# Kernel tuning notes

Hardware: AMD Instinct MI355X
Metric: run time of the kernel (lower is better)

The kernel has to match this reference:

```python
import jax, jax.numpy as jnp
import numpy as np

B, S, DIM = 1, 2048, 1024
HEADS, KV_HEADS, DH = 16, 2, 64
GQ = HEADS // KV_HEADS
CBS = 64   # compress block size
SBS = 64   # selection block size
NUM_SEL = 8
WIN = 512  # sliding window size
NUM_MEM = 1
SCALE = DH ** -0.5
NEG = -jnp.finfo(jnp.float32).max


def setup_inputs():
    ks = jax.random.split(jax.random.key(0), 12)
    cdim = CBS * DH
    dim_inner = HEADS * DH
    dim_kv = KV_HEADS * DH
    p = lambda k, shape: jax.random.normal(k, shape, jnp.float32) * 0.02
    return {
        "x": jax.random.normal(ks[0], (B, S, DIM), jnp.float32),
        "rms_g": jnp.ones((DIM,), jnp.float32),
        "W_qkv": p(ks[1], (DIM, dim_inner + 2 * dim_kv)),
        "k_pos": p(ks[2], (KV_HEADS, CBS, DH)),
        "v_pos": p(ks[3], (KV_HEADS, CBS, DH)),
        "mem_kv": p(ks[4], (2, KV_HEADS, NUM_MEM, DH)),
        "kW1": p(ks[5], (cdim, cdim)), "kb1": jnp.zeros((cdim,), jnp.float32),
        "kW2": p(ks[6], (cdim, DH)), "kb2": jnp.zeros((DH,), jnp.float32),
        "vW1": p(ks[7], (cdim, cdim)), "vb1": jnp.zeros((cdim,), jnp.float32),
        "vW2": p(ks[8], (cdim, DH)), "vb2": jnp.zeros((DH,), jnp.float32),
        "W_comb": p(ks[9], (DIM, 3 * HEADS)),
        "b_comb": jnp.tile(jnp.array([-2.0, -2.0, 2.0], jnp.float32), HEADS),
        "W_out": p(ks[10], (HEADS * DH, DIM)),
    }


def _rot_half(u):
    v = u.reshape(u.shape[:-1] + (DH // 2, 2))
    return jnp.stack([-v[..., 1], v[..., 0]], axis=-1).reshape(u.shape)


def reference(x, rms_g, W_qkv, k_pos, v_pos, mem_kv, kW1, kb1, kW2, kb2,
              vW1, vb1, vW2, vb2, W_comb, b_comb, W_out):
    n_cb = S // CBS
    n_fb = S // SBS
    num_sel = min(NUM_SEL, n_cb)

    # RMSNorm
    xn = x * jax.lax.rsqrt(jnp.mean(x * x, -1, keepdims=True) + jnp.finfo(jnp.float32).eps) * rms_g

    qkv = xn @ W_qkv
    q, k, v = jnp.split(qkv, [HEADS * DH, (HEADS + KV_HEADS) * DH], axis=-1)
    q = q.reshape(B, S, HEADS, DH).transpose(0, 2, 1, 3)       # b h n d
    k = k.reshape(B, S, KV_HEADS, DH).transpose(0, 2, 1, 3)
    v = v.reshape(B, S, KV_HEADS, DH).transpose(0, 2, 1, 3)

    # ---- compressed branch: per-block MLP compression of K/V ----
    kc = (k + jnp.tile(k_pos, (1, n_cb, 1))[None]).reshape(B, KV_HEADS, n_cb, CBS * DH)
    vc = (v + jnp.tile(v_pos, (1, n_cb, 1))[None]).reshape(B, KV_HEADS, n_cb, CBS * DH)
    ck = jax.nn.relu(kc @ kW1 + kb1) @ kW2 + kb2               # b h w d
    cv = jax.nn.relu(vc @ vW1 + vb1) @ vW2 + vb2
    ck = jnp.concatenate([jnp.broadcast_to(mem_kv[0], (B, KV_HEADS, NUM_MEM, DH)), ck], axis=2)
    cv = jnp.concatenate([jnp.broadcast_to(mem_kv[1], (B, KV_HEADS, NUM_MEM, DH)), cv], axis=2)
    ck_seq = jnp.concatenate([jnp.full((NUM_MEM,), -1), (jnp.arange(n_cb) + 1) * CBS - 1])
    cmask = ck_seq[None, :] < jnp.arange(S)[:, None]           # [S, mem+n_cb]
    qg = q.reshape(B, KV_HEADS, GQ, S, DH)
    csim = jnp.einsum('bhgid,bhjd->bhgij', qg, ck) * SCALE
    csim = jnp.where(cmask, csim, NEG)
    c_out = jnp.einsum('bhgij,bhjd->bhgid', jax.nn.softmax(csim, -1), cv).reshape(B, HEADS, S, DH)

    # ---- rotary embedding (interleaved pairs, theta=10000) ----
    inv_freq = 1.0 / (10000.0 ** (jnp.arange(0, DH, 2, dtype=jnp.float32) / DH))
    freqs = jnp.repeat(jnp.arange(S, dtype=jnp.float32)[:, None] * inv_freq, 2, axis=-1)
    cos, sin = jnp.cos(freqs), jnp.sin(freqs)
    rq = q * cos + _rot_half(q) * sin
    rk = k * cos + _rot_half(k) * sin

    # ---- block selection from compressed attention scores ----
    imp = csim[..., NUM_MEM:].mean(axis=2)                     # mean over grouped queries: [B,KVH,S,n_cb]
    imp = jnp.concatenate([jnp.full(imp.shape[:-1] + (1,), -1000.0), imp], -1)
    imp = jax.nn.softmax(imp, -1)[..., 1:]
    sel_val, sel_idx = jax.lax.top_k(imp, num_sel)             # [B,KVH,S,sel]
    fmask = jnp.broadcast_to((sel_val > 1e-10)[..., None], (B, KV_HEADS, S, num_sel, SBS))
    diag_idx = jnp.broadcast_to((jnp.arange(S) // SBS)[None, None, :, None], (B, KV_HEADS, S, 1))
    sel_idx = jnp.concatenate([sel_idx, diag_idx], -1)         # append own (diagonal) block
    causal = jnp.tril(jnp.ones((SBS, SBS), bool))
    diag_mask = jnp.broadcast_to(jnp.tile(causal, (n_fb, 1))[None, None, :, None, :], (B, KV_HEADS, S, 1, SBS))
    fmask = jnp.concatenate([fmask, diag_mask], axis=-2).reshape(B, KV_HEADS, S, (num_sel + 1) * SBS)

    # ---- fine attention over gathered selected blocks ----
    fkb = rk.reshape(B, KV_HEADS, 1, n_fb, SBS, DH)
    fvb = v.reshape(B, KV_HEADS, 1, n_fb, SBS, DH)
    gi = sel_idx[..., None, None]                              # [B,KVH,S,sel+1,1,1]
    fk = jnp.take_along_axis(fkb, gi, axis=3).reshape(B, KV_HEADS, S, (num_sel + 1) * SBS, DH)
    fv = jnp.take_along_axis(fvb, gi, axis=3).reshape(B, KV_HEADS, S, (num_sel + 1) * SBS, DH)
    fqg = rq.reshape(B, KV_HEADS, GQ, S, DH)
    fsim = jnp.einsum('bhgid,bhijd->bhgij', fqg, fk) * SCALE
    fsim = jnp.where(fmask[:, :, None], fsim, NEG)
    f_out = jnp.einsum('bhgij,bhijd->bhgid', jax.nn.softmax(fsim, -1), fv).reshape(B, HEADS, S, DH)

    # ---- causal sliding window (exact window, look_backward=1) ----
    skf = jnp.repeat(rk, GQ, axis=1)
    svf = jnp.repeat(v, GQ, axis=1)
    nw = S // WIN
    kw = skf.reshape(B, HEADS, nw, WIN, DH)
    vw = svf.reshape(B, HEADS, nw, WIN, DH)
    kcat = jnp.concatenate([jnp.pad(kw, ((0, 0), (0, 0), (1, 0), (0, 0), (0, 0)))[:, :, :nw], kw], axis=3)
    vcat = jnp.concatenate([jnp.pad(vw, ((0, 0), (0, 0), (1, 0), (0, 0), (0, 0)))[:, :, :nw], vw], axis=3)
    qw = rq.reshape(B, HEADS, nw, WIN, DH)
    gq_pos = jnp.arange(nw)[:, None, None] * WIN + jnp.arange(WIN)[None, :, None]
    gk_pos = jnp.arange(nw)[:, None, None] * WIN - WIN + jnp.arange(2 * WIN)[None, None, :]
    smask = (gk_pos >= 0) & (gk_pos <= gq_pos) & (gq_pos - gk_pos <= WIN)
    ssim = jnp.where(smask, jnp.einsum('bhwid,bhwjd->bhwij', qw, kcat) * SCALE, NEG)
    s_out = jnp.einsum('bhwij,bhwjd->bhwid', jax.nn.softmax(ssim, -1), vcat).reshape(B, HEADS, S, DH)

    # ---- learned per-token, per-head strategy combination ----
    gates = jax.nn.sigmoid(xn @ W_comb + b_comb).reshape(B, S, HEADS, 3).transpose(0, 2, 1, 3)
    out = gates[..., 0:1] * c_out + gates[..., 1:2] * f_out + gates[..., 2:3] * s_out
    return out.transpose(0, 2, 1, 3).reshape(B, S, HEADS * DH) @ W_out
```

## Files before the change

### kernel.cpp

```cpp
#include <hip/hip_runtime.h>
#include <hip/hip_bf16.h>
#include <cstddef>
#include <cstdint>

#define S      2048
#define DIM    1024
#define HEADS  16
#define KVH    2
#define GQ     8
#define DH     64
#define CBS    64
#define SBS    64
#define NUMSEL 8
#define WIN    512
#define NCB    (S / CBS)
#define CDIM   (CBS * DH)
#define QKVC   (HEADS * DH + 2 * KVH * DH)
#define KOFF   (HEADS * DH)
#define VOFF   (HEADS * DH + KVH * DH)
#define SCALE  0.125f
#define RMS_EPS 1.1920928955078125e-07f

typedef __attribute__((ext_vector_type(8))) short bf16x8;
typedef __attribute__((ext_vector_type(4))) float f32x4;

__device__ inline short f2bs(float f) {
    __hip_bfloat16 b = __float2bfloat16(f);
    return *(short*)&b;
}

__device__ inline float wave_sum(float v) {
    for (int o = 32; o > 0; o >>= 1) v += __shfl_xor(v, o);
    return v;
}

__global__ __launch_bounds__(256) void rmsnorm_kernel(
        const float* __restrict__ x, const float* __restrict__ g,
        float* __restrict__ xn, __hip_bfloat16* __restrict__ xnb) {
    int s = blockIdx.x, tid = threadIdx.x;
    const float4* row = (const float4*)(x + (size_t)s * DIM);
    float4 v = row[tid];
    float ss = v.x * v.x + v.y * v.y + v.z * v.z + v.w * v.w;
    ss = wave_sum(ss);
    __shared__ float red[4];
    if ((tid & 63) == 0) red[tid >> 6] = ss;
    __syncthreads();
    float tot = red[0] + red[1] + red[2] + red[3];
    float sc = rsqrtf(tot / (float)DIM + RMS_EPS);
    float4 gg = ((const float4*)g)[tid];
    float4 o;
    o.x = v.x * sc * gg.x; o.y = v.y * sc * gg.y;
    o.z = v.z * sc * gg.z; o.w = v.w * sc * gg.w;
    ((float4*)(xn + (size_t)s * DIM))[tid] = o;
    size_t b = (size_t)s * DIM + tid * 4;
    xnb[b + 0] = __float2bfloat16(o.x);
    xnb[b + 1] = __float2bfloat16(o.y);
    xnb[b + 2] = __float2bfloat16(o.z);
    xnb[b + 3] = __float2bfloat16(o.w);
}

__global__ __launch_bounds__(256) void cast_bf16_kernel(
        const float* __restrict__ in, __hip_bfloat16* __restrict__ out, int n4) {
    int e = blockIdx.x * 256 + threadIdx.x;
    if (e >= n4) return;
    float4 v = ((const float4*)in)[e];
    out[4 * e + 0] = __float2bfloat16(v.x);
    out[4 * e + 1] = __float2bfloat16(v.y);
    out[4 * e + 2] = __float2bfloat16(v.z);
    out[4 * e + 3] = __float2bfloat16(v.w);
}

__global__ __launch_bounds__(256) void transpose_cast_kernel(
        const float* __restrict__ W, short* __restrict__ Wt, int K, int N) {
    __shared__ float tile[64][65];
    int n0 = blockIdx.x * 64, k0 = blockIdx.y * 64;
    int tid = threadIdx.x;
    #pragma unroll
    for (int e = 0; e < 16; e++) {
        int idx = tid + e * 256;
        int r = idx >> 6, c = idx & 63;
        float v = 0.f;
        if (n0 + c < N) v = W[(size_t)(k0 + r) * N + n0 + c];
        tile[r][c] = v;
    }
    __syncthreads();
    #pragma unroll
    for (int e = 0; e < 16; e++) {
        int idx = tid + e * 256;
        int r = idx >> 6, c = idx & 63;
        if (n0 + r < N)
            Wt[(size_t)(n0 + r) * K + k0 + c] = f2bs(tile[c][r]);
    }
}

__global__ __launch_bounds__(256) void transpose_v_kernel(
        const float* __restrict__ qkv, short* __restrict__ vtg) {
    int k0 = blockIdx.x * 64, kvh = blockIdx.y;
    __shared__ float tile[64][65];
    int tid = threadIdx.x;
    #pragma unroll
    for (int e = 0; e < 16; e++) {
        int idx = tid + e * 256;
        int key = idx >> 6, d = idx & 63;
        tile[key][d] = qkv[(size_t)(k0 + key) * QKVC + VOFF + kvh * DH + d];
    }
    __syncthreads();
    #pragma unroll
    for (int e = 0; e < 16; e++) {
        int idx = tid + e * 256;
        int d = idx >> 6, key = idx & 63;
        vtg[(size_t)(kvh * DH + d) * S + k0 + key] = f2bs(tile[key][d]);
    }
}

template <int BM, int BN, int WM, int WN, int ACT>
__global__ __launch_bounds__(256) void gemm_bt_kernel(
        const __hip_bfloat16* __restrict__ A, const short* __restrict__ Bt,
        const float* __restrict__ bias, float* __restrict__ C,
        int M, int N, int K) {
    constexpr int BK = 32;
    constexpr int TM = BM / (WM * 16);
    constexpr int TN = BN / (WN * 16);
    constexpr int LDK = BK + 8;
    __shared__ short As[BM][LDK];
    __shared__ short Bs[BN][LDK];
    int tid = threadIdx.x;
    int wave = tid >> 6, lane = tid & 63;
    int wm = wave % WM, wn = wave / WM;
    int m0 = wm * TM * 16, n0 = wn * TN * 16;
    int bm = blockIdx.y * BM, bn = blockIdx.x * BN;
    int lm = lane & 15, quad = lane >> 4;
    const short* Ash = (const short*)A;
    f32x4 acc[TM][TN] = {};
    for (int k0 = 0; k0 < K; k0 += BK) {
        #pragma unroll
        for (int e = 0; e < BM * BK / (256 * 8); e++) {
            int idx = (tid + e * 256) * 8;
            int r = idx >> 5, kk = idx & 31;
            *(bf16x8*)(&As[r][kk]) =
                *(const bf16x8*)(Ash + (size_t)(bm + r) * K + k0 + kk);
        }
        #pragma unroll
        for (int e = 0; e < BN * BK / (256 * 8); e++) {
            int idx = (tid + e * 256) * 8;
            int r = idx >> 5, kk = idx & 31;
            bf16x8 v = {};
            if (bn + r < N)
                v = *(const bf16x8*)(Bt + (size_t)(bn + r) * K + k0 + kk);
            *(bf16x8*)(&Bs[r][kk]) = v;
        }
        __syncthreads();
        bf16x8 af[TM], bf_[TN];
        #pragma unroll
        for (int i = 0; i < TM; i++)
            af[i] = *(const bf16x8*)(&As[m0 + i * 16 + lm][quad * 8]);
        #pragma unroll
        for (int j = 0; j < TN; j++)
            bf_[j] = *(const bf16x8*)(&Bs[n0 + j * 16 + lm][quad * 8]);
        #pragma unroll
        for (int i = 0; i < TM; i++)
            #pragma unroll
            for (int j = 0; j < TN; j++)
                acc[i][j] = __builtin_amdgcn_mfma_f32_16x16x32_bf16(
                    af[i], bf_[j], acc[i][j], 0, 0, 0);
        __syncthreads();
    }
    #pragma unroll
    for (int i = 0; i < TM; i++) {
        #pragma unroll
        for (int j = 0; j < TN; j++) {
            int gn = bn + n0 + j * 16 + lm;
            if (gn >= N) continue;
            #pragma unroll
            for (int r = 0; r < 4; r++) {
                int gm = bm + m0 + i * 16 + quad * 4 + r;
                float v = acc[i][j][r];
                if (bias) v += bias[gn];
                if (ACT == 2) v = 1.f / (1.f + expf(-v));
                C[(size_t)gm * N + gn] = v;
            }
        }
    }
}

template <int BM, int BN, int WM, int WN>
__global__ __launch_bounds__(256) void gemm_mfma_kernel(
        const __hip_bfloat16* __restrict__ A, const float* __restrict__ B,
        float* __restrict__ C, int M, int N, int K, int kslice) {
    constexpr int BK = 32;
    constexpr int TM = BM / (WM * 16);
    constexpr int TN = BN / (WN * 16);
    constexpr int LDK = BK + 8;
    constexpr int NB = BN * BK / 256;
    __shared__ __hip_bfloat16 As[BM][LDK];
    __shared__ __hip_bfloat16 Bs[BN][LDK];
    int tid = threadIdx.x;
    int wave = tid >> 6, lane = tid & 63;
    int wm = wave % WM, wn = wave / WM;
    int m0 = wm * TM * 16, n0 = wn * TN * 16;
    int bm = blockIdx.y * BM, bn = blockIdx.x * BN;
    int kbeg = blockIdx.z * kslice, kend = kbeg + kslice;
    int lm = lane & 15, quad = lane >> 4;
    f32x4 acc[TM][TN] = {};
    for (int k0 = kbeg; k0 < kend; k0 += BK) {
        #pragma unroll
        for (int e = 0; e < BM * BK / (256 * 8); e++) {
            int idx = (tid + e * 256) * 8;
            int r = idx >> 5, kk = idx & 31;
            *(bf16x8*)(&As[r][kk]) =
                *(const bf16x8*)(A + (size_t)(bm + r) * K + k0 + kk);
        }
        float tmpB[NB];
        #pragma unroll
        for (int e = 0; e < NB; e++) {
            int idx = tid + e * 256;
            int kk = idx / BN, n = idx % BN;
            tmpB[e] = B[(size_t)(k0 + kk) * N + bn + n];
        }
        #pragma unroll
        for (int e = 0; e < NB; e++) {
            int idx = tid + e * 256;
            int kk = idx / BN, n = idx % BN;
            Bs[n][kk] = __float2bfloat16(tmpB[e]);
        }
        __syncthreads();
        bf16x8 af[TM], bf_[TN];
        #pragma unroll
        for (int i = 0; i < TM; i++)
            af[i] = *(const bf16x8*)(&As[m0 + i * 16 + lm][quad * 8]);
        #pragma unroll
        for (int j = 0; j < TN; j++)
            bf_[j] = *(const bf16x8*)(&Bs[n0 + j * 16 + lm][quad * 8]);
        #pragma unroll
        for (int i = 0; i < TM; i++)
            #pragma unroll
            for (int j = 0; j < TN; j++)
                acc[i][j] = __builtin_amdgcn_mfma_f32_16x16x32_bf16(
                    af[i], bf_[j], acc[i][j], 0, 0, 0);
        __syncthreads();
    }
    size_t cbase = (size_t)blockIdx.z * M * N;
    #pragma unroll
    for (int i = 0; i < TM; i++) {
        #pragma unroll
        for (int j = 0; j < TN; j++) {
            int gn = bn + n0 + j * 16 + lm;
            #pragma unroll
            for (int r = 0; r < 4; r++) {
                int gm = bm + m0 + i * 16 + quad * 4 + r;
                C[cbase + (size_t)gm * N + gn] = acc[i][j][r];
            }
        }
    }
}

__global__ __launch_bounds__(256) void gemm_splitk_kernel(
        const float* __restrict__ A, const float* __restrict__ B,
        float* __restrict__ P, int M, int N, int K, int kslice) {
    const int BM = 64, BN = 64, BK = 16;
    __shared__ float As[BK][BM + 4];
    __shared__ float Bs[BK][BN];
    int bm = blockIdx.y * BM, bn = blockIdx.x * BN;
    int z = blockIdx.z;
    int kbeg = z * kslice, kend = kbeg + kslice;
    int tid = threadIdx.x;
    int tx = tid & 15, ty = tid >> 4;
    float acc[4][4] = {{0.f}};
    for (int k0 = kbeg; k0 < kend; k0 += BK) {
        #pragma unroll
        for (int e = 0; e < 4; e++) {
            int idx = tid + e * 256;
            int m = idx >> 4, kk = idx & 15;
            int gm = bm + m;
            As[kk][m] = (gm < M) ? A[(size_t)gm * K + k0 + kk] : 0.f;
        }
        #pragma unroll
        for (int e = 0; e < 4; e++) {
            int idx = tid + e * 256;
            int kk = idx >> 6, n = idx & 63;
            int gn = bn + n;
            Bs[kk][n] = (gn < N) ? B[(size_t)(k0 + kk) * N + gn] : 0.f;
        }
        __syncthreads();
        #pragma unroll
        for (int kk = 0; kk < BK; kk++) {
            float a[4], b[4];
            #pragma unroll
            for (int i = 0; i < 4; i++) a[i] = As[kk][ty * 4 + i];
            #pragma unroll
            for (int j = 0; j < 4; j++) b[j] = Bs[kk][tx * 4 + j];
            #pragma unroll
            for (int i = 0; i < 4; i++)
                #pragma unroll
                for (int j = 0; j < 4; j++) acc[i][j] += a[i] * b[j];
        }
        __syncthreads();
    }
    #pragma unroll
    for (int i = 0; i < 4; i++) {
        int gm = bm + ty * 4 + i;
        if (gm >= M) continue;
        #pragma unroll
        for (int j = 0; j < 4; j++) {
            int gn = bn + tx * 4 + j;
            if (gn >= N) continue;
            P[((size_t)z * M + gm) * N + gn] = acc[i][j];
        }
    }
}

template <int ACT>
__global__ __launch_bounds__(256) void reduce_splitk_kernel(
        const float* __restrict__ P, const float* __restrict__ bias,
        float* __restrict__ C, int MN, int N, int splits) {
    int e = blockIdx.x * 256 + threadIdx.x;
    if (e >= MN) return;
    float s = 0.f;
    for (int z = 0; z < splits; z++) s += P[(size_t)z * MN + e];
    s += bias[e % N];
    if (ACT == 1) s = fmaxf(s, 0.f);
    C[e] = s;
}

__global__ __launch_bounds__(256) void rotary_kernel(
        const float* __restrict__ qkv, short* __restrict__ rqb, short* __restrict__ rkb) {
    int s = blockIdx.x, tid = threadIdx.x;
    for (int p = tid; p < (HEADS + KVH) * (DH / 2); p += 256) {
        int t; const float* src; short* dst;
        if (p < HEADS * (DH / 2)) {
            int h = p >> 5; t = p & 31;
            src = qkv + (size_t)s * QKVC + h * DH + 2 * t;
            dst = rqb + (size_t)s * (HEADS * DH) + h * DH + 2 * t;
        } else {
            int pp = p - HEADS * (DH / 2);
            int h = pp >> 5; t = pp & 31;
            src = qkv + (size_t)s * QKVC + KOFF + h * DH + 2 * t;
            dst = rkb + (size_t)s * (KVH * DH) + h * DH + 2 * t;
        }
        float u0 = src[0], u1 = src[1];
        float freq = powf(10000.f, -((float)(2 * t) / (float)DH));
        float ang = (float)s * freq;
        float sn, cs;
        sincosf(ang, &sn, &cs);
        dst[0] = f2bs(u0 * cs - u1 * sn);
        dst[1] = f2bs(u1 * cs + u0 * sn);
    }
}

__global__ __launch_bounds__(256) void build_cmat_kernel(
        const float* __restrict__ qkv, const float* __restrict__ k_pos,
        const float* __restrict__ v_pos, __hip_bfloat16* __restrict__ kcm,
        __hip_bfloat16* __restrict__ vcm) {
    int r = blockIdx.x;
    int h = r >> 5, w = r & 31;
    for (int e = threadIdx.x; e < CDIM; e += 256) {
        int i = e >> 6, d = e & 63;
        size_t qb = (size_t)(w * CBS + i) * QKVC;
        kcm[(size_t)r * CDIM + e] =
            __float2bfloat16(qkv[qb + KOFF + h * DH + d] + k_pos[(h * CBS + i) * DH + d]);
        vcm[(size_t)r * CDIM + e] =
            __float2bfloat16(qkv[qb + VOFF + h * DH + d] + v_pos[(h * CBS + i) * DH + d]);
    }
}

__global__ __launch_bounds__(256) void assemble_kernel(
        const float* __restrict__ ckb, const float* __restrict__ cvb,
        const float* __restrict__ mem_kv, float* __restrict__ ck, float* __restrict__ cv,
        short* __restrict__ ck16, short* __restrict__ cv16) {
    int e = blockIdx.x * 256 + threadIdx.x;
    if (e >= KVH * (NCB + 1) * DH) return;
    int d = e & 63;
    int j = (e >> 6) % (NCB + 1);
    int h = e / ((NCB + 1) * DH);
    float kv, vv;
    if (j == 0) {
        kv = mem_kv[0 * KVH * DH + h * DH + d];
        vv = mem_kv[1 * KVH * DH + h * DH + d];
    } else {
        kv = ckb[((size_t)h * NCB + j - 1) * DH + d];
        vv = cvb[((size_t)h * NCB + j - 1) * DH + d];
    }
    ck[e] = kv; cv[e] = vv;
    ck16[e] = f2bs(kv); cv16[e] = f2bs(vv);
}

__global__ __launch_bounds__(64) void imp_kernel(
        const float* __restrict__ qkv, const float* __restrict__ ck,
        float* __restrict__ imp) {
    int kvh = blockIdx.x, s = blockIdx.y, t = threadIdx.x;
    __shared__ float qg[GQ * DH];
    __shared__ float ckl[NCB * 65];
    for (int e = t; e < GQ * DH; e += 64) {
        int g = e >> 6, d = e & 63;
        qg[e] = qkv[(size_t)s * QKVC + (kvh * GQ + g) * DH + d];
    }
    for (int e = t; e < NCB * DH; e += 64) {
        int w = e >> 6, d = e & 63;
        ckl[w * 65 + d] = ck[((size_t)kvh * (NCB + 1) + 1 + w) * DH + d];
    }
    __syncthreads();
    if (t < NCB) {
        int w = t;
        float val;
        if (w * CBS + CBS - 1 < s) {
            float acc = 0.f;
            #pragma unroll
            for (int g = 0; g < GQ; g++) {
                const float* qp = qg + g * DH;
                const float* cp = ckl + w * 65;
                #pragma unroll 16
                for (int d = 0; d < DH; d++) acc += qp[d] * cp[d];
            }
            val = acc * SCALE * (1.f / (float)GQ);
        } else {
            val = -INFINITY;
        }
        imp[((size_t)kvh * S + s) * NCB + w] = val;
    }
}

__global__ __launch_bounds__(256) void select_kernel(
        const float* __restrict__ imp, int* __restrict__ sel) {
    int idx = blockIdx.x * 256 + threadIdx.x;
    if (idx >= KVH * S) return;
    const float* row = imp + (size_t)idx * NCB;
    float p[NCB];
    float m = -1000.f;
    for (int w = 0; w < NCB; w++) { p[w] = row[w]; m = fmaxf(m, p[w]); }
    float z = expf(-1000.f - m);
    for (int w = 0; w < NCB; w++) { p[w] = expf(p[w] - m); z += p[w]; }
    float inv = 1.f / z;
    bool used[NCB];
    for (int w = 0; w < NCB; w++) used[w] = false;
    for (int i = 0; i < NUMSEL; i++) {
        int best = 0; float bv = -1.f;
        for (int w = 0; w < NCB; w++) {
            if (!used[w]) {
                float pw = p[w] * inv;
                if (pw > bv) { bv = pw; best = w; }
            }
        }
        used[best] = true;
        sel[(size_t)idx * NUMSEL + i] = (bv > 1e-10f) ? best : -1;
    }
}

__global__ __launch_bounds__(256) void cattn_kernel(
        const float* __restrict__ qkv, const short* __restrict__ ck16,
        const short* __restrict__ cv16, const float* __restrict__ gates,
        float* __restrict__ attn) {
    int h = blockIdx.x, qb = blockIdx.y;
    int kvh = h >> 3;
    int tid = threadIdx.x;
    int wv = tid >> 6, lane = tid & 63;
    int lm = lane & 15, quad = lane >> 4;
    __shared__ short Qb[64][72];
    __shared__ short Ks[64][72];
    __shared__ short Vt[64][72];
    __shared__ short Pb[64][72];
    for (int e = tid; e < 1024; e += 256) {
        int q = e >> 4, d4 = (e & 15) * 4;
        float4 v = *(const float4*)(qkv + (size_t)(qb * 64 + q) * QKVC + h * DH + d4);
        Qb[q][d4 + 0] = f2bs(v.x); Qb[q][d4 + 1] = f2bs(v.y);
        Qb[q][d4 + 2] = f2bs(v.z); Qb[q][d4 + 3] = f2bs(v.w);
    }
    for (int e = tid; e < 512; e += 256) {
        int c8 = e >> 6, j = e & 63;
        bf16x8 kv = {}, vv = {};
        if (j < NCB + 1) {
            kv = *(const bf16x8*)(ck16 + ((size_t)kvh * (NCB + 1) + j) * DH + c8 * 8);
            vv = *(const bf16x8*)(cv16 + ((size_t)kvh * (NCB + 1) + j) * DH + c8 * 8);
        }
        #pragma unroll
        for (int t = 0; t < 8; t++) {
            Ks[j][c8 * 8 + t] = kv[t];
            Vt[c8 * 8 + t][j] = vv[t];
        }
    }
    __syncthreads();
    bf16x8 aq0 = *(const bf16x8*)&Qb[wv * 16 + lm][quad * 8];
    bf16x8 aq1 = *(const bf16x8*)&Qb[wv * 16 + lm][32 + quad * 8];
    int vismax = (qb < NCB) ? qb : NCB;
    f32x4 sc[4];
    #pragma unroll
    for (int t = 0; t < 4; t++) {
        bf16x8 bk0 = *(const bf16x8*)&Ks[t * 16 + lm][quad * 8];
        bf16x8 bk1 = *(const bf16x8*)&Ks[t * 16 + lm][32 + quad * 8];
        f32x4 s4 = {0.f, 0.f, 0.f, 0.f};
        s4 = __builtin_amdgcn_mfma_f32_16x16x32_bf16(aq0, bk0, s4, 0, 0, 0);
        s4 = __builtin_amdgcn_mfma_f32_16x16x32_bf16(aq1, bk1, s4, 0, 0, 0);
        sc[t] = s4;
    }
    float l[4];
    float pr[4][4];
    #pragma unroll
    for (int r = 0; r < 4; r++) {
        float mx = -INFINITY;
        #pragma unroll
        for (int t = 0; t < 4; t++) {
            int jj = t * 16 + lm;
            bool vis = (jj == 0) || (jj <= vismax);
            float v = vis ? sc[t][r] * SCALE : -INFINITY;
            sc[t][r] = v;
            mx = fmaxf(mx, v);
        }
        #pragma unroll
        for (int o = 1; o < 16; o <<= 1) mx = fmaxf(mx, __shfl_xor(mx, o));
        float sum = 0.f;
        #pragma unroll
        for (int t = 0; t < 4; t++) {
            float p = __expf(sc[t][r] - mx);
            pr[r][t] = p;
            sum += p;
        }
        #pragma unroll
        for (int o = 1; o < 16; o <<= 1) sum += __shfl_xor(sum, o);
        l[r] = sum;
    }
    #pragma unroll
    for (int r = 0; r < 4; r++)
        #pragma unroll
        for (int t = 0; t < 4; t++)
            Pb[wv * 16 + quad * 4 + r][t * 16 + lm] = f2bs(pr[r][t]);
    __syncthreads();
    bf16x8 ap0 = *(const bf16x8*)&Pb[wv * 16 + lm][quad * 8];
    bf16x8 ap1 = *(const bf16x8*)&Pb[wv * 16 + lm][32 + quad * 8];
    f32x4 oacc[4];
    #pragma unroll
    for (int t = 0; t < 4; t++) {
        bf16x8 bv0 = *(const bf16x8*)&Vt[t * 16 + lm][quad * 8];
        bf16x8 bv1 = *(const bf16x8*)&Vt[t * 16 + lm][32 + quad * 8];
        f32x4 a = {0.f, 0.f, 0.f, 0.f};
        a = __builtin_amdgcn_mfma_f32_16x16x32_bf16(ap0, bv0, a, 0, 0, 0);
        a = __builtin_amdgcn_mfma_f32_16x16x32_bf16(ap1, bv1, a, 0, 0, 0);
        oacc[t] = a;
    }
    #pragma unroll
    for (int r = 0; r < 4; r++) {
        int spos = qb * 64 + wv * 16 + quad * 4 + r;
        float g0 = gates[((size_t)spos * HEADS + h) * 3 + 0];
        float f = g0 / l[r];
        #pragma unroll
        for (int t = 0; t < 4; t++)
            attn[(size_t)spos * (HEADS * DH) + h * DH + t * 16 + lm] = oacc[t][r] * f;
    }
}

__global__ __launch_bounds__(256) void fattn_kernel(
        const short* __restrict__ rqb, const short* __restrict__ rkb,
        const short* __restrict__ vtg, const int* __restrict__ sel,
        const float* __restrict__ gates, float* __restrict__ attn) {
    int kvh = blockIdx.x;
    int tid = threadIdx.x;
    int wv = tid >> 6, lane = tid & 63;
    int s = blockIdx.y * 4 + wv;
    int lm = lane & 15, quad = lane >> 4;
    __shared__ short Pb[4][16][68];
    short (*Pw)[68] = Pb[wv];
    const short* qp = rqb + (size_t)s * (HEADS * DH) + (size_t)(kvh * 8 + (lm & 7)) * DH;
    bf16x8 aq0 = *(const bf16x8*)(qp + quad * 8);
    bf16x8 aq1 = *(const bf16x8*)(qp + 32 + quad * 8);
    const short* vrow[4];
    #pragma unroll
    for (int t = 0; t < 4; t++)
        vrow[t] = vtg + (size_t)(kvh * DH + t * 16 + lm) * S;
    int bl[9];
    {
        const int4* sp = (const int4*)(sel + ((size_t)kvh * S + s) * NUMSEL);
        int4 s0 = sp[0], s1 = sp[1];
        bl[0] = s0.x; bl[1] = s0.y; bl[2] = s0.z; bl[3] = s0.w;
        bl[4] = s1.x; bl[5] = s1.y; bl[6] = s1.z; bl[7] = s1.w;
        bl[8] = s >> 6;
    }
    float m[4], l[4];
    f32x4 oacc[4];
    #pragma unroll
    for (int r = 0; r < 4; r++) {
        m[r] = -INFINITY; l[r] = 0.f;
        oacc[r] = (f32x4){0.f, 0.f, 0.f, 0.f};
    }
    for (int i = 0; i < 9; i++) {
        int w = bl[i];
        if (i < NUMSEL && w < 0) continue;
        bf16x8 bv0[4], bv1[4];
        #pragma unroll
        for (int t = 0; t < 4; t++) {
            bv0[t] = *(const bf16x8*)(vrow[t] + w * SBS + quad * 8);
            bv1[t] = *(const bf16x8*)(vrow[t] + w * SBS + 32 + quad * 8);
        }
        f32x4 sc[4];
        #pragma unroll
        for (int t = 0; t < 4; t++) {
            const short* kp = rkb + ((size_t)(w * SBS + t * 16 + lm) * KVH + kvh) * DH;
            bf16x8 bk0 = *(const bf16x8*)(kp + quad * 8);
            bf16x8 bk1 = *(const bf16x8*)(kp + 32 + quad * 8);
            f32x4 s4 = {0.f, 0.f, 0.f, 0.f};
            s4 = __builtin_amdgcn_mfma_f32_16x16x32_bf16(aq0, bk0, s4, 0, 0, 0);
            s4 = __builtin_amdgcn_mfma_f32_16x16x32_bf16(aq1, bk1, s4, 0, 0, 0);
            sc[t] = s4;
        }
        bool diag = (i == 8);
        #pragma unroll
        for (int r = 0; r < 4; r++) {
            float mx = -INFINITY;
            #pragma unroll
            for (int t = 0; t < 4; t++) {
                int jj = t * 16 + lm;
                bool vis = !diag || (jj <= (s & 63));
                float v = vis ? sc[t][r] * SCALE : -INFINITY;
                sc[t][r] = v;
                mx = fmaxf(mx, v);
            }
            #pragma unroll
            for (int o = 1; o < 16; o <<= 1) mx = fmaxf(mx, __shfl_xor(mx, o));
            float mn = fmaxf(m[r], mx);
            float al = __expf(m[r] - mn);
            float sum = 0.f;
            #pragma unroll
            for (int t = 0; t < 4; t++) {
                float pv_ = __expf(sc[t][r] - mn);
                sc[t][r] = pv_;
                sum += pv_;
            }
            #pragma unroll
            for (int o = 1; o < 16; o <<= 1) sum += __shfl_xor(sum, o);
            l[r] = l[r] * al + sum;
            m[r] = mn;
            #pragma unroll
            for (int t = 0; t < 4; t++) oacc[t][r] *= al;
        }
        #pragma unroll
        for (int r = 0; r < 4; r++)
            #pragma unroll
            for (int t = 0; t < 4; t++)
                Pw[quad * 4 + r][t * 16 + lm] = f2bs(sc[t][r]);
        asm volatile("s_waitcnt lgkmcnt(0)" ::: "memory");
        bf16x8 ap0 = *(const bf16x8*)&Pw[lm][quad * 8];
        bf16x8 ap1 = *(const bf16x8*)&Pw[lm][32 + quad * 8];
        #pragma unroll
        for (int t = 0; t < 4; t++) {
            oacc[t] = __builtin_amdgcn_mfma_f32_16x16x32_bf16(ap0, bv0[t], oacc[t], 0, 0, 0);
            oacc[t] = __builtin_amdgcn_mfma_f32_16x16x32_bf16(ap1, bv1[t], oacc[t], 0, 0, 0);
        }
    }
    if (quad < 2) {
        #pragma unroll
        for (int r = 0; r < 4; r++) {
            int head = kvh * 8 + quad * 4 + r;
            float fac = gates[((size_t)s * HEADS + head) * 3 + 1] / l[r];
            #pragma unroll
            for (int t = 0; t < 4; t++)
                attn[(size_t)s * (HEADS * DH) + head * DH + t * 16 + lm]
                    += oacc[t][r] * fac;
        }
    }
}

__global__ __launch_bounds__(256) void sattn_kernel(
        const short* __restrict__ rqb, const short* __restrict__ rkb,
        const short* __restrict__ vtg, const float* __restrict__ gates,
        float* __restrict__ attn) {
    int h = blockIdx.x;
    int kvh = h >> 3;
    int tid = threadIdx.x;
    int wv = tid >> 6, lane = tid & 63;
    int q0 = blockIdx.y * 64 + wv * 16;
    int lm = lane & 15, quad = lane >> 4;
    __shared__ short Pb[4][16][68];
    short (*Pw)[68] = Pb[wv];
    const short* qp = rqb + (size_t)(q0 + lm) * (HEADS * DH) + h * DH;
    bf16x8 aq0 = *(const bf16x8*)(qp + quad * 8);
    bf16x8 aq1 = *(const bf16x8*)(qp + 32 + quad * 8);
    const short* vrow[4];
    #pragma unroll
    for (int t = 0; t < 4; t++)
        vrow[t] = vtg + (size_t)(kvh * DH + t * 16 + lm) * S;
    int myrow = quad * 4;
    float m[4], l[4];
    f32x4 oacc[4];
    #pragma unroll
    for (int r = 0; r < 4; r++) { m[r] = -INFINITY; l[r] = 0.f; }
    #pragma unroll
    for (int t = 0; t < 4; t++) oacc[t] = (f32x4){0.f, 0.f, 0.f, 0.f};
    int kb_start = ((q0 - WIN) >> 6) << 6;
    for (int kb = kb_start; kb <= q0 + 15; kb += 64) {
        if (kb < 0) continue;
        bf16x8 bv0[4], bv1[4];
        #pragma unroll
        for (int t = 0; t < 4; t++) {
            bv0[t] = *(const bf16x8*)(vrow[t] + kb + quad * 8);
            bv1[t] = *(const bf16x8*)(vrow[t] + kb + 32 + quad * 8);
        }
        f32x4 sc[4];
        #pragma unroll
        for (int t = 0; t < 4; t++) {
            const short* kp = rkb + ((size_t)(kb + t * 16 + lm) * KVH + kvh) * DH;
            bf16x8 bk0 = *(const bf16x8*)(kp + quad * 8);
            bf16x8 bk1 = *(const bf16x8*)(kp + 32 + quad * 8);
            f32x4 s4 = {0.f, 0.f, 0.f, 0.f};
            s4 = __builtin_amdgcn_mfma_f32_16x16x32_bf16(aq0, bk0, s4, 0, 0, 0);
            s4 = __builtin_amdgcn_mfma_f32_16x16x32_bf16(aq1, bk1, s4, 0, 0, 0);
            sc[t] = s4;
        }
        #pragma unroll
        for (int r = 0; r < 4; r++) {
            int gq = q0 + myrow + r;
            float mx = -INFINITY;
            #pragma unroll
            for (int t = 0; t < 4; t++) {
                int jjg = kb + t * 16 + lm;
                bool vis = (jjg <= gq) && (gq - jjg <= WIN);
                float v = vis ? sc[t][r] * SCALE : -INFINITY;
                sc[t][r] = v;
                mx = fmaxf(mx, v);
            }
            #pragma unroll
            for (int o = 1; o < 16; o <<= 1) mx = fmaxf(mx, __shfl_xor(mx, o));
            float mn = fmaxf(m[r], mx);
            float al = __expf(m[r] - mn);
            float sum = 0.f;
            #pragma unroll
            for (int t = 0; t < 4; t++) {
                float pv_ = __expf(sc[t][r] - mn);
                sc[t][r] = pv_;
                sum += pv_;
            }
            #pragma unroll
            for (int o = 1; o < 16; o <<= 1) sum += __shfl_xor(sum, o);
            l[r] = l[r] * al + sum;
            m[r] = mn;
            #pragma unroll
            for (int t = 0; t < 4; t++) oacc[t][r] *= al;
        }
        #pragma unroll
        for (int r = 0; r < 4; r++)
            #pragma unroll
            for (int t = 0; t < 4; t++)
                Pw[myrow + r][t * 16 + lm] = f2bs(sc[t][r]);
        asm volatile("s_waitcnt lgkmcnt(0)" ::: "memory");
        bf16x8 ap0 = *(const bf16x8*)&Pw[lm][quad * 8];
        bf16x8 ap1 = *(const bf16x8*)&Pw[lm][32 + quad * 8];
        #pragma unroll
        for (int t = 0; t < 4; t++) {
            oacc[t] = __builtin_amdgcn_mfma_f32_16x16x32_bf16(ap0, bv0[t], oacc[t], 0, 0, 0);
            oacc[t] = __builtin_amdgcn_mfma_f32_16x16x32_bf16(ap1, bv1[t], oacc[t], 0, 0, 0);
        }
    }
    #pragma unroll
    for (int r = 0; r < 4; r++) {
        int spos = q0 + myrow + r;
        float g2 = gates[((size_t)spos * HEADS + h) * 3 + 2];
        float f = g2 / l[r];
        #pragma unroll
        for (int t = 0; t < 4; t++)
            attn[(size_t)spos * (HEADS * DH) + h * DH + t * 16 + lm] += oacc[t][r] * f;
    }
}

extern "C" void kernel_launch(void* const* d_in, const int* in_sizes, int n_in,
                              void* d_out, int out_size, void* d_ws, size_t ws_size,
                              hipStream_t stream) {
    const float* x      = (const float*)d_in[0];
    const float* rms_g  = (const float*)d_in[1];
    const float* W_qkv  = (const float*)d_in[2];
    const float* k_pos  = (const float*)d_in[3];
    const float* v_pos  = (const float*)d_in[4];
    const float* mem_kv = (const float*)d_in[5];
    const float* kW1    = (const float*)d_in[6];
    const float* kb1    = (const float*)d_in[7];
    const float* kW2    = (const float*)d_in[8];
    const float* kb2    = (const float*)d_in[9];
    const float* vW1    = (const float*)d_in[10];
    const float* vb1    = (const float*)d_in[11];
    const float* vW2    = (const float*)d_in[12];
    const float* vb2    = (const float*)d_in[13];
    const float* W_comb = (const float*)d_in[14];
    const float* b_comb = (const float*)d_in[15];
    const float* W_out  = (const float*)d_in[16];
    float* out = (float*)d_out;

    float* ws    = (float*)d_ws;
    float* xn    = ws;
    float* qkv   = xn    + (size_t)S * DIM;
    short* rqb   = (short*)(qkv + (size_t)S * QKVC);
    short* rkb   = (short*)((float*)rqb + 1048576);
    float* R     = (float*)rkb + 131072;
    float* ck    = R     + 1048576;
    float* cv    = ck    + (size_t)KVH * (NCB + 1) * DH;
    short* ck16  = (short*)(cv + (size_t)KVH * (NCB + 1) * DH);
    short* cv16  = (short*)((float*)ck16 + 2112);
    float* imp   = (float*)cv16 + 2112;
    float* gates = imp   + (size_t)KVH * S * NCB;
    float* attn  = gates + (size_t)S * HEADS * 3;
    int*   sel   = (int*)(attn + (size_t)S * HEADS * DH);
    float* WT    = attn + (size_t)S * HEADS * DH + 8192;
    short* wqkvT = (short*)WT;
    short* woutT = (short*)(WT + 655360);
    short* wcombT= (short*)(WT + 655360 + 524288);

    __hip_bfloat16* xnb   = (__hip_bfloat16*)R;
    __hip_bfloat16* kcmb  = (__hip_bfloat16*)R;
    __hip_bfloat16* vcmb  = (__hip_bfloat16*)(R + 131072);
    float* khid  = R + 262144;
    float* vhid  = R + 524288;
    float* ckb   = R + 786432;
    float* cvb   = R + 790528;
    __hip_bfloat16* attnb = (__hip_bfloat16*)R;
    short* vtg   = (short*)imp;
    float* partW1 = attn;
    float* partW2 = imp;

    transpose_cast_kernel<<<dim3(QKVC / 64, DIM / 64), 256, 0, stream>>>(W_qkv, wqkvT, DIM, QKVC);
    transpose_cast_kernel<<<dim3(DIM / 64, DIM / 64), 256, 0, stream>>>(W_out, woutT, DIM, DIM);
    transpose_cast_kernel<<<dim3(1, DIM / 64), 256, 0, stream>>>(W_comb, wcombT, DIM, HEADS * 3);
    rmsnorm_kernel<<<S, 256, 0, stream>>>(x, rms_g, xn, xnb);
    gemm_bt_kernel<64, 64, 2, 2, 0><<<dim3(QKVC / 64, S / 64), 256, 0, stream>>>(
        xnb, wqkvT, nullptr, qkv, S, QKVC, DIM);
    gemm_bt_kernel<64, 64, 2, 2, 2><<<dim3(1, S / 64), 256, 0, stream>>>(
        xnb, wcombT, b_comb, gates, S, HEADS * 3, DIM);
    rotary_kernel<<<S, 256, 0, stream>>>(qkv, rqb, rkb);
    build_cmat_kernel<<<KVH * NCB, 256, 0, stream>>>(qkv, k_pos, v_pos, kcmb, vcmb);
    gemm_mfma_kernel<64, 128, 1, 4><<<dim3(CDIM / 128, 1, 8), 256, 0, stream>>>(
        kcmb, kW1, partW1, 64, CDIM, CDIM, CDIM / 8);
    reduce_splitk_kernel<1><<<(64 * CDIM + 255) / 256, 256, 0, stream>>>(
        partW1, kb1, khid, 64 * CDIM, CDIM, 8);
    gemm_splitk_kernel<<<dim3(1, 1, 32), 256, 0, stream>>>(khid, kW2, partW2, 64, DH, CDIM, CDIM / 32);
    reduce_splitk_kernel<0><<<(64 * DH + 255) / 256, 256, 0, stream>>>(partW2, kb2, ckb, 64 * DH, DH, 32);
    gemm_mfma_kernel<64, 128, 1, 4><<<dim3(CDIM / 128, 1, 8), 256, 0, stream>>>(
        vcmb, vW1, partW1, 64, CDIM, CDIM, CDIM / 8);
    reduce_splitk_kernel<1><<<(64 * CDIM + 255) / 256, 256, 0, stream>>>(
        partW1, vb1, vhid, 64 * CDIM, CDIM, 8);
    gemm_splitk_kernel<<<dim3(1, 1, 32), 256, 0, stream>>>(vhid, vW2, partW2, 64, DH, CDIM, CDIM / 32);
    reduce_splitk_kernel<0><<<(64 * DH + 255) / 256, 256, 0, stream>>>(partW2, vb2, cvb, 64 * DH, DH, 32);
    assemble_kernel<<<(KVH * (NCB + 1) * DH + 255) / 256, 256, 0, stream>>>(
        ckb, cvb, mem_kv, ck, cv, ck16, cv16);
    imp_kernel<<<dim3(KVH, S), 64, 0, stream>>>(qkv, ck, imp);
    select_kernel<<<(KVH * S + 255) / 256, 256, 0, stream>>>(imp, sel);
    transpose_v_kernel<<<dim3(S / 64, KVH), 256, 0, stream>>>(qkv, vtg);
    cattn_kernel<<<dim3(HEADS, S / 64), 256, 0, stream>>>(qkv, ck16, cv16, gates, attn);
    fattn_kernel<<<dim3(KVH, S / 4), 256, 0, stream>>>(rqb, rkb, vtg, sel, gates, attn);
    sattn_kernel<<<dim3(HEADS, S / 64), 256, 0, stream>>>(rqb, rkb, vtg, gates, attn);
    cast_bf16_kernel<<<(S * HEADS * DH / 4 + 255) / 256, 256, 0, stream>>>(
        attn, attnb, S * HEADS * DH / 4);
    gemm_bt_kernel<64, 64, 2, 2, 0><<<dim3(DIM / 64, S / 64), 256, 0, stream>>>(
        attnb, woutT, nullptr, out, S, DIM, DIM);
}
```

Measured before the change: 543.8 us.

## Fuse three attention branch kernels into one launch with atomic accumulation

Merges the compressed, fine-selection and sliding-window attention kernels into a single kernel that dispatches on block index. Each block runs one branch, so the branches can occupy the GPU concurrently instead of running as three serial launches. Because outputs now race, each branch accumulates with float atomicAdd into a buffer zeroed by a memset first. This adds atomic traffic and a memset pass, and the summation order becomes nondeterministic.

```diff
diff --git a/kernel.cpp b/kernel.cpp
--- a/kernel.cpp
+++ b/kernel.cpp
@@ -445,19 +445,15 @@
     }
 }
 
-__global__ __launch_bounds__(256) void cattn_kernel(
+
+__device__ __forceinline__ void cattn_body(
         const float* __restrict__ qkv, const short* __restrict__ ck16,
         const short* __restrict__ cv16, const float* __restrict__ gates,
-        float* __restrict__ attn) {
-    int h = blockIdx.x, qb = blockIdx.y;
+        float* __restrict__ attn, int h, int qb, int tid,
+        short (*Qb)[72], short (*Ks)[72], short (*Vt)[72], short (*Pb)[72]) {
     int kvh = h >> 3;
-    int tid = threadIdx.x;
     int wv = tid >> 6, lane = tid & 63;
     int lm = lane & 15, quad = lane >> 4;
-    __shared__ short Qb[64][72];
-    __shared__ short Ks[64][72];
-    __shared__ short Vt[64][72];
-    __shared__ short Pb[64][72];
     for (int e = tid; e < 1024; e += 256) {
         int q = e >> 4, d4 = (e & 15) * 4;
         float4 v = *(const float4*)(qkv + (size_t)(qb * 64 + q) * QKVC + h * DH + d4);
@@ -542,21 +538,17 @@
         float f = g0 / l[r];
         #pragma unroll
         for (int t = 0; t < 4; t++)
-            attn[(size_t)spos * (HEADS * DH) + h * DH + t * 16 + lm] = oacc[t][r] * f;
-    }
-}
-
-__global__ __launch_bounds__(256) void fattn_kernel(
+            atomicAdd(&attn[(size_t)spos * (HEADS * DH) + h * DH + t * 16 + lm],
+                      oacc[t][r] * f);
+    }
+}
+
+__device__ __forceinline__ void fattn_body(
         const short* __restrict__ rqb, const short* __restrict__ rkb,
         const short* __restrict__ vtg, const int* __restrict__ sel,
-        const float* __restrict__ gates, float* __restrict__ attn) {
-    int kvh = blockIdx.x;
-    int tid = threadIdx.x;
-    int wv = tid >> 6, lane = tid & 63;
-    int s = blockIdx.y * 4 + wv;
+        const float* __restrict__ gates, float* __restrict__ attn,
+        int kvh, int s, int lane, short (*Pw)[68]) {
     int lm = lane & 15, quad = lane >> 4;
-    __shared__ short Pb[4][16][68];
-    short (*Pw)[68] = Pb[wv];
     const short* qp = rqb + (size_t)s * (HEADS * DH) + (size_t)(kvh * 8 + (lm & 7)) * DH;
     bf16x8 aq0 = *(const bf16x8*)(qp + quad * 8);
     bf16x8 aq1 = *(const bf16x8*)(qp + 32 + quad * 8);
@@ -650,24 +642,18 @@
             float fac = gates[((size_t)s * HEADS + head) * 3 + 1] / l[r];
             #pragma unroll
             for (int t = 0; t < 4; t++)
-                attn[(size_t)s * (HEADS * DH) + head * DH + t * 16 + lm]
-                    += oacc[t][r] * fac;
-        }
-    }
-}
-
-__global__ __launch_bounds__(256) void sattn_kernel(
+                atomicAdd(&attn[(size_t)s * (HEADS * DH) + head * DH + t * 16 + lm],
+                          oacc[t][r] * fac);
+        }
+    }
+}
+
+__device__ __forceinline__ void sattn_body(
         const short* __restrict__ rqb, const short* __restrict__ rkb,
         const short* __restrict__ vtg, const float* __restrict__ gates,
-        float* __restrict__ attn) {
-    int h = blockIdx.x;
+        float* __restrict__ attn, int h, int q0, int lane, short (*Pw)[68]) {
     int kvh = h >> 3;
-    int tid = threadIdx.x;
-    int wv = tid >> 6, lane = tid & 63;
-    int q0 = blockIdx.y * 64 + wv * 16;
     int lm = lane & 15, quad = lane >> 4;
-    __shared__ short Pb[4][16][68];
-    short (*Pw)[68] = Pb[wv];
     const short* qp = rqb + (size_t)(q0 + lm) * (HEADS * DH) + h * DH;
     bf16x8 aq0 = *(const bf16x8*)(qp + quad * 8);
     bf16x8 aq1 = *(const bf16x8*)(qp + 32 + quad * 8);
@@ -753,7 +739,34 @@
         float f = g2 / l[r];
         #pragma unroll
         for (int t = 0; t < 4; t++)
-            attn[(size_t)spos * (HEADS * DH) + h * DH + t * 16 + lm] += oacc[t][r] * f;
+            atomicAdd(&attn[(size_t)spos * (HEADS * DH) + h * DH + t * 16 + lm],
+                      oacc[t][r] * f);
+    }
+}
+
+__global__ __launch_bounds__(256) void fused_attn_kernel(
+        const float* __restrict__ qkv, const short* __restrict__ ck16,
+        const short* __restrict__ cv16, const short* __restrict__ rqb,
+        const short* __restrict__ rkb, const short* __restrict__ vtg,
+        const int* __restrict__ sel, const float* __restrict__ gates,
+        float* __restrict__ attn) {
+    __shared__ short smem[4][64][72];
+    int bid = blockIdx.x;
+    int t4 = bid & 3, sub = bid >> 2;
+    int tid = threadIdx.x;
+    int wv = tid >> 6, lane = tid & 63;
+    if (t4 == 2) {
+        cattn_body(qkv, ck16, cv16, gates, attn, sub & 15, sub >> 4, tid,
+                   smem[0], smem[1], smem[2], smem[3]);
+    } else if (t4 == 3) {
+        short (*Pw)[68] = (short(*)[68])(&smem[0][0][0] + wv * 16 * 68);
+        sattn_body(rqb, rkb, vtg, gates, attn, sub & 15, (sub >> 4) * 64 + wv * 16,
+                   lane, Pw);
+    } else {
+        int f = sub * 2 + t4;
+        short (*Pw)[68] = (short(*)[68])(&smem[0][0][0] + wv * 16 * 68);
+        fattn_body(rqb, rkb, vtg, sel, gates, attn, f & 1, (f >> 1) * 4 + wv,
+                   lane, Pw);
     }
 }
 
@@ -837,9 +850,9 @@
     imp_kernel<<<dim3(KVH, S), 64, 0, stream>>>(qkv, ck, imp);
     select_kernel<<<(KVH * S + 255) / 256, 256, 0, stream>>>(imp, sel);
     transpose_v_kernel<<<dim3(S / 64, KVH), 256, 0, stream>>>(qkv, vtg);
-    cattn_kernel<<<dim3(HEADS, S / 64), 256, 0, stream>>>(qkv, ck16, cv16, gates, attn);
-    fattn_kernel<<<dim3(KVH, S / 4), 256, 0, stream>>>(rqb, rkb, vtg, sel, gates, attn);
-    sattn_kernel<<<dim3(HEADS, S / 64), 256, 0, stream>>>(rqb, rkb, vtg, gates, attn);
+    hipMemsetAsync(attn, 0, (size_t)S * HEADS * DH * sizeof(float), stream);
+    fused_attn_kernel<<<2048, 256, 0, stream>>>(
+        qkv, ck16, cv16, rqb, rkb, vtg, sel, gates, attn);
     cast_bf16_kernel<<<(S * HEADS * DH / 4 + 255) / 256, 256, 0, stream>>>(
         attn, attnb, S * HEADS * DH / 4);
     gemm_bt_kernel<64, 64, 2, 2, 0><<<dim3(DIM / 64, S / 64), 256, 0, stream>>>(
```

Result: slower. 559.7 us (+2.9%).
